# Optimization experiments

Measured on AMD Instinct MI355X. Metric: run time of the kernel, lower is better.

The kernel has to match this reference:

```python
import jax, jax.numpy as jnp
import numpy as np

MEM_DIM = 1024
N_CHILD = 16384

def _linear_params(key, out_dim, in_dim):
    kw, kb = jax.random.split(key)
    bound = 1.0 / np.sqrt(in_dim)
    W = jax.random.uniform(kw, (out_dim, in_dim), jnp.float32, -bound, bound)
    b = jax.random.uniform(kb, (out_dim,), jnp.float32, -bound, bound)
    return W, b

def setup_inputs() -> dict:
    key = jax.random.key(0)
    ks = jax.random.split(key, 7)
    child_c = jax.random.normal(ks[0], (N_CHILD, MEM_DIM), jnp.float32)
    child_h = jax.random.normal(ks[1], (N_CHILD, MEM_DIM), jnp.float32)
    child_h_sum = jax.random.normal(ks[2], (MEM_DIM,), jnp.float32)
    W_ih, b_ih = _linear_params(ks[3], MEM_DIM, MEM_DIM)
    W_fh, b_fh = _linear_params(ks[4], MEM_DIM, MEM_DIM)
    W_uh, b_uh = _linear_params(ks[5], MEM_DIM, MEM_DIM)
    W_oh, b_oh = _linear_params(ks[6], MEM_DIM, MEM_DIM)
    return {
        "child_c": child_c, "child_h": child_h, "child_h_sum": child_h_sum,
        "W_ih": W_ih, "b_ih": b_ih, "W_fh": W_fh, "b_fh": b_fh,
        "W_uh": W_uh, "b_uh": b_uh, "W_oh": W_oh, "b_oh": b_oh,
    }

def reference(child_c, child_h, child_h_sum,
              W_ih, b_ih, W_fh, b_fh, W_uh, b_uh, W_oh, b_oh):
    # Gate projections on the summed child hidden state: [mem_dim]
    i = jax.nn.sigmoid(child_h_sum @ W_ih.T + b_ih)
    o = jax.nn.sigmoid(child_h_sum @ W_oh.T + b_oh)
    u = jnp.tanh(child_h_sum @ W_uh.T + b_uh)
    # Per-child forget gates, batched (replaces the Python loop): [N, mem_dim]
    f = jax.nn.sigmoid(child_h @ W_fh.T + b_fh)
    fc = f * child_c                     # [N, mem_dim]
    c = i * u + jnp.sum(fc, axis=0)      # [mem_dim]
    h = o * jnp.tanh(c)                  # [mem_dim]
    return (c, h)
```

## Files before the change

kernel.cpp:

```cpp
#include <hip/hip_runtime.h>
#include <hip/hip_bf16.h>
#include <math.h>

#define MEM_DIM 1024
#define N_CHILD 16384

typedef __bf16 bf16_t;
typedef __bf16 bf16x4 __attribute__((ext_vector_type(4)));
typedef __bf16 bf16x8 __attribute__((ext_vector_type(8)));
typedef float f32x4 __attribute__((ext_vector_type(4)));

__device__ __forceinline__ void async_load16(const bf16_t* g, bf16_t* l) {
    __builtin_amdgcn_global_load_lds(
        (const __attribute__((address_space(1))) unsigned int*)g,
        (__attribute__((address_space(3))) unsigned int*)l,
        16, 0, 0);
}

template<int N> __device__ __forceinline__ void wait_vm() {
    if constexpr (N == 0)      asm volatile("s_waitcnt vmcnt(0)" ::: "memory");
    else if constexpr (N == 4) asm volatile("s_waitcnt vmcnt(4)" ::: "memory");
    else if constexpr (N == 8) asm volatile("s_waitcnt vmcnt(8)" ::: "memory");
}

__device__ __forceinline__ void block_barrier() {
    __builtin_amdgcn_sched_barrier(0);
    asm volatile("" ::: "memory");
    __builtin_amdgcn_s_barrier();
    asm volatile("" ::: "memory");
    __builtin_amdgcn_sched_barrier(0);
}

__global__ __launch_bounds__(256) void prep_kernel(
        const float* __restrict__ child_h, const float* __restrict__ W_fh,
        bf16_t* __restrict__ dst, int n8,
        const float* __restrict__ hsum,
        const float* __restrict__ W_ih, const float* __restrict__ b_ih,
        const float* __restrict__ W_uh, const float* __restrict__ b_uh,
        const float* __restrict__ W_oh, const float* __restrict__ b_oh,
        float* __restrict__ acc_c, float* __restrict__ o_ws) {
    const int tid = threadIdx.x;
    if (blockIdx.x < MEM_DIM) {
        const int j = blockIdx.x;
        const float* wi = W_ih + (size_t)j * MEM_DIM;
        const float* wu = W_uh + (size_t)j * MEM_DIM;
        const float* wo = W_oh + (size_t)j * MEM_DIM;
        float4 h4  = *(const float4*)(hsum + tid * 4);
        float4 wi4 = *(const float4*)(wi + tid * 4);
        float4 wu4 = *(const float4*)(wu + tid * 4);
        float4 wo4 = *(const float4*)(wo + tid * 4);
        float si = wi4.x * h4.x + wi4.y * h4.y + wi4.z * h4.z + wi4.w * h4.w;
        float su = wu4.x * h4.x + wu4.y * h4.y + wu4.z * h4.z + wu4.w * h4.w;
        float so = wo4.x * h4.x + wo4.y * h4.y + wo4.z * h4.z + wo4.w * h4.w;
        for (int off = 32; off > 0; off >>= 1) {
            si += __shfl_down(si, off, 64);
            su += __shfl_down(su, off, 64);
            so += __shfl_down(so, off, 64);
        }
        __shared__ float red[3][4];
        const int wave = tid >> 6, lane = tid & 63;
        if (lane == 0) { red[0][wave] = si; red[1][wave] = su; red[2][wave] = so; }
        __syncthreads();
        if (tid == 0) {
            float ti = red[0][0] + red[0][1] + red[0][2] + red[0][3] + b_ih[j];
            float tu = red[1][0] + red[1][1] + red[1][2] + red[1][3] + b_uh[j];
            float to = red[2][0] + red[2][1] + red[2][2] + red[2][3] + b_oh[j];
            float iv = 1.f / (1.f + expf(-ti));
            float uv = tanhf(tu);
            float ov = 1.f / (1.f + expf(-to));
            acc_c[j] = iv * uv;
            o_ws[j]  = ov;
        }
    } else {
        const int nA8 = (N_CHILD * MEM_DIM) / 8;
        int t = (blockIdx.x - MEM_DIM) * 256 + tid;
        if (t < n8) {
            const float* s = (t < nA8) ? (child_h + (size_t)t * 8)
                                       : (W_fh + (size_t)(t - nA8) * 8);
            float4 a = *(const float4*)s;
            float4 b = *(const float4*)(s + 4);
            bf16x8 o = { (bf16_t)a.x, (bf16_t)a.y, (bf16_t)a.z, (bf16_t)a.w,
                         (bf16_t)b.x, (bf16_t)b.y, (bf16_t)b.z, (bf16_t)b.w };
            *(bf16x8*)(dst + (size_t)t * 8) = o;
        }
    }
}


__device__ __forceinline__ void stage_slot(const bf16_t* __restrict__ gbase,
                                           int row0, int s, bf16_t* lds_slot,
                                           int tid) {
    const int wave = tid >> 6;
    const int rr   = tid >> 2;
    const int cf   = ((tid & 3) ^ (rr & 3)) * 8;
#pragma unroll
    for (int i = 0; i < 2; ++i) {
        const bf16_t* src = gbase + (size_t)(row0 + i * 128 + rr) * MEM_DIM
                          + s * 32 + cf;
        bf16_t* dst = lds_slot + i * 4096 + wave * 512;
        async_load16(src, dst);
    }
}

template<int VMN, bool STG>
__device__ __forceinline__ void do_slice(
        int s, bf16_t* ldsA, bf16_t* ldsB,
        const bf16_t* __restrict__ hbf, const bf16_t* __restrict__ wbf,
        int n0, int j0, int tid, int wr, int wc, int q, int cl,
        f32x4 (&acc)[8][4]) {
    const int m = s & 3;
    const int koff  = (q ^ (cl & 3)) * 8;
    const int abase = m * 8192 + (wr * 128 + cl) * 32 + koff;
    const int bbase = m * 8192 + (wc * 64  + cl) * 32 + koff;
    bf16x8 af[8], bfr[2];

#pragma unroll
    for (int mt = 0; mt < 8; ++mt)
        af[mt] = *(const bf16x8*)(&ldsA[abase + mt * 512]);
#pragma unroll
    for (int nt = 0; nt < 2; ++nt)
        bfr[nt] = *(const bf16x8*)(&ldsB[bbase + nt * 512]);
    if (STG) stage_slot(hbf, n0, s + 3, ldsA + ((s + 3) & 3) * 8192, tid);
    block_barrier();
    asm volatile("s_waitcnt lgkmcnt(0)" ::: "memory");
    __builtin_amdgcn_sched_barrier(0);
    __builtin_amdgcn_s_setprio(1);
#pragma unroll
    for (int mt = 0; mt < 8; ++mt) {
        acc[mt][0] = __builtin_amdgcn_mfma_f32_16x16x32_bf16(af[mt], bfr[0], acc[mt][0], 0, 0, 0);
        acc[mt][1] = __builtin_amdgcn_mfma_f32_16x16x32_bf16(af[mt], bfr[1], acc[mt][1], 0, 0, 0);
    }
    __builtin_amdgcn_s_setprio(0);
    block_barrier();

#pragma unroll
    for (int nt = 0; nt < 2; ++nt)
        bfr[nt] = *(const bf16x8*)(&ldsB[bbase + (2 + nt) * 512]);
    if (STG) stage_slot(wbf, j0, s + 3, ldsB + ((s + 3) & 3) * 8192, tid);
    if constexpr (VMN >= 0) wait_vm<VMN>();
    block_barrier();
    asm volatile("s_waitcnt lgkmcnt(0)" ::: "memory");
    __builtin_amdgcn_sched_barrier(0);
    __builtin_amdgcn_s_setprio(1);
#pragma unroll
    for (int mt = 0; mt < 8; ++mt) {
        acc[mt][2] = __builtin_amdgcn_mfma_f32_16x16x32_bf16(af[mt], bfr[0], acc[mt][2], 0, 0, 0);
        acc[mt][3] = __builtin_amdgcn_mfma_f32_16x16x32_bf16(af[mt], bfr[1], acc[mt][3], 0, 0, 0);
    }
    __builtin_amdgcn_s_setprio(0);
    block_barrier();
}

__global__ __launch_bounds__(512, 2) void gemm8_kernel(
        const bf16_t* __restrict__ hbf, const bf16_t* __restrict__ wbf,
        const float* __restrict__ child_c, const float* __restrict__ b_fh,
        float* __restrict__ acc_part) {
    __shared__ __align__(1024) bf16_t ldsA[4 * 8192];
    __shared__ __align__(1024) bf16_t ldsB[4 * 8192];
    __shared__ float sred[256];

    const int tid  = threadIdx.x;
    const int lane = tid & 63;
    const int wave = tid >> 6;
    const int wr = wave >> 2;
    const int wc = wave & 3;
    const int q  = lane >> 4;
    const int cl = lane & 15;

    const int b   = blockIdx.x;
    const int xcd = b & 7;
    const int l   = b >> 3;
    const int jt  = l & 3;
    const int ntl = l >> 2;
    const int j0  = jt * 256;
    const int n0  = (xcd * 8 + ntl) * 256;
    const int part = xcd * 8 + ntl;

    f32x4 acc[8][4];
#pragma unroll
    for (int a = 0; a < 8; ++a)
#pragma unroll
        for (int c = 0; c < 4; ++c) acc[a][c] = (f32x4)0.0f;

#pragma unroll
    for (int s = 0; s < 3; ++s) {
        stage_slot(hbf, n0, s, ldsA + (s & 3) * 8192, tid);
        stage_slot(wbf, j0, s, ldsB + (s & 3) * 8192, tid);
    }
    wait_vm<8>();
    block_barrier();

#pragma unroll 1
    for (int s = 0; s < 29; ++s)
        do_slice<8, true>(s, ldsA, ldsB, hbf, wbf, n0, j0, tid, wr, wc, q, cl, acc);
    do_slice<4,  false>(29, ldsA, ldsB, hbf, wbf, n0, j0, tid, wr, wc, q, cl, acc);
    do_slice<0,  false>(30, ldsA, ldsB, hbf, wbf, n0, j0, tid, wr, wc, q, cl, acc);
    do_slice<-1, false>(31, ldsA, ldsB, hbf, wbf, n0, j0, tid, wr, wc, q, cl, acc);

    float colsum[4] = {0.f, 0.f, 0.f, 0.f};
#pragma unroll
    for (int nt = 0; nt < 4; ++nt) {
        const int j = j0 + wc * 64 + nt * 16 + cl;
        const float bias = b_fh[j];
#pragma unroll
        for (int mt = 0; mt < 8; ++mt) {
            const int nrow = n0 + wr * 128 + mt * 16 + q * 4;
            const float* ccp = child_c + (size_t)nrow * MEM_DIM + j;
#pragma unroll
            for (int rr = 0; rr < 4; ++rr) {
                float sv = acc[mt][nt][rr] + bias;
                float fg = 1.0f / (1.0f + __expf(-sv));
                colsum[nt] += fg * ccp[(size_t)rr * MEM_DIM];
            }
        }
        colsum[nt] += __shfl_xor(colsum[nt], 16, 64);
        colsum[nt] += __shfl_xor(colsum[nt], 32, 64);
    }
    if (tid < 256) sred[tid] = 0.0f;
    __syncthreads();
    if (q == 0) {
#pragma unroll
        for (int nt = 0; nt < 4; ++nt)
            atomicAdd(&sred[wc * 64 + nt * 16 + cl], colsum[nt]);
    }
    __syncthreads();
    if (tid < 256)
        acc_part[(size_t)part * MEM_DIM + j0 + tid] = sred[tid];
}

__global__ __launch_bounds__(256) void finalize2(
        const float* __restrict__ acc_part, const float* __restrict__ iu_ws,
        const float* __restrict__ o_ws, float* __restrict__ out) {
    const int j = blockIdx.x * 256 + threadIdx.x;
    float s = iu_ws[j];
#pragma unroll 8
    for (int p = 0; p < 64; ++p)
        s += acc_part[(size_t)p * MEM_DIM + j];
    out[j] = s;
    out[MEM_DIM + j] = o_ws[j] * tanhf(s);
}

__global__ void gates_kernel(const float* __restrict__ hsum,
                             const float* __restrict__ W_ih, const float* __restrict__ b_ih,
                             const float* __restrict__ W_uh, const float* __restrict__ b_uh,
                             const float* __restrict__ W_oh, const float* __restrict__ b_oh,
                             float* __restrict__ acc_c, float* __restrict__ o_ws) {
    const int j = blockIdx.x;
    const int tid = threadIdx.x;
    const float* wi = W_ih + (size_t)j * MEM_DIM;
    const float* wu = W_uh + (size_t)j * MEM_DIM;
    const float* wo = W_oh + (size_t)j * MEM_DIM;
    float si = 0.f, su = 0.f, so = 0.f;
    for (int k = tid; k < MEM_DIM; k += 256) {
        float hv = hsum[k];
        si += wi[k] * hv;
        su += wu[k] * hv;
        so += wo[k] * hv;
    }
    for (int off = 32; off > 0; off >>= 1) {
        si += __shfl_down(si, off, 64);
        su += __shfl_down(su, off, 64);
        so += __shfl_down(so, off, 64);
    }
    __shared__ float red[3][4];
    const int wave = tid >> 6, lane = tid & 63;
    if (lane == 0) { red[0][wave] = si; red[1][wave] = su; red[2][wave] = so; }
    __syncthreads();
    if (tid == 0) {
        float ti = red[0][0] + red[0][1] + red[0][2] + red[0][3] + b_ih[j];
        float tu = red[1][0] + red[1][1] + red[1][2] + red[1][3] + b_uh[j];
        float to = red[2][0] + red[2][1] + red[2][2] + red[2][3] + b_oh[j];
        acc_c[j] = (1.f / (1.f + expf(-ti))) * tanhf(tu);
        o_ws[j]  = 1.f / (1.f + expf(-to));
    }
}

#define LDS_STRIDE 40
__global__ __launch_bounds__(256) void fused_gemm_f32(
        const float* __restrict__ child_h, const float* __restrict__ child_c,
        const float* __restrict__ W_fh, const float* __restrict__ b_fh,
        float* __restrict__ acc_c) {
    __shared__ __align__(16) bf16_t sA[128 * LDS_STRIDE];
    __shared__ __align__(16) bf16_t sB[128 * LDS_STRIDE];
    __shared__ float sred[128];
    const int tid = threadIdx.x, lane = tid & 63, wave = tid >> 6;
    const int wr = wave >> 1, wc = wave & 1;
    const int j0 = blockIdx.x * 128, n0 = blockIdx.y * 128;
    const int q = lane >> 4, cl = lane & 15;
    f32x4 acc[4][4];
#pragma unroll
    for (int a = 0; a < 4; a++)
#pragma unroll
        for (int c = 0; c < 4; c++) acc[a][c] = (f32x4)0.0f;
    for (int k0 = 0; k0 < MEM_DIM; k0 += 32) {
#pragma unroll
        for (int i = 0; i < 4; i++) {
            int f = tid + i * 256, row = f >> 3, col = (f & 7) * 4;
            float4 va = *(const float4*)(child_h + (size_t)(n0 + row) * MEM_DIM + k0 + col);
            float4 vb = *(const float4*)(W_fh    + (size_t)(j0 + row) * MEM_DIM + k0 + col);
            bf16x4 ba = { (bf16_t)va.x, (bf16_t)va.y, (bf16_t)va.z, (bf16_t)va.w };
            bf16x4 bb = { (bf16_t)vb.x, (bf16_t)vb.y, (bf16_t)vb.z, (bf16_t)vb.w };
            *(bf16x4*)(&sA[row * LDS_STRIDE + col]) = ba;
            *(bf16x4*)(&sB[row * LDS_STRIDE + col]) = bb;
        }
        __syncthreads();
        bf16x8 af[4], bfr[4];
#pragma unroll
        for (int mt = 0; mt < 4; mt++) {
            af[mt]  = *(const bf16x8*)(&sA[(wr * 64 + mt * 16 + cl) * LDS_STRIDE + q * 8]);
            bfr[mt] = *(const bf16x8*)(&sB[(wc * 64 + mt * 16 + cl) * LDS_STRIDE + q * 8]);
        }
#pragma unroll
        for (int mt = 0; mt < 4; mt++)
#pragma unroll
            for (int nt = 0; nt < 4; nt++)
                acc[mt][nt] = __builtin_amdgcn_mfma_f32_16x16x32_bf16(af[mt], bfr[nt], acc[mt][nt], 0, 0, 0);
        __syncthreads();
    }
    if (tid < 128) sred[tid] = 0.0f;
    __syncthreads();
    float colsum[4] = {0.f, 0.f, 0.f, 0.f};
#pragma unroll
    for (int nt = 0; nt < 4; nt++) {
        const int col = j0 + wc * 64 + nt * 16 + cl;
        const float bias = b_fh[col];
#pragma unroll
        for (int mt = 0; mt < 4; mt++)
#pragma unroll
            for (int r = 0; r < 4; r++) {
                const int row = n0 + wr * 64 + mt * 16 + q * 4 + r;
                float s = acc[mt][nt][r] + bias;
                float fg = 1.0f / (1.0f + __expf(-s));
                colsum[nt] += fg * child_c[(size_t)row * MEM_DIM + col];
            }
        colsum[nt] += __shfl_xor(colsum[nt], 16, 64);
        colsum[nt] += __shfl_xor(colsum[nt], 32, 64);
    }
    if (q == 0)
#pragma unroll
        for (int nt = 0; nt < 4; nt++)
            atomicAdd(&sred[wc * 64 + nt * 16 + cl], colsum[nt]);
    __syncthreads();
    if (tid < 128) atomicAdd(&acc_c[j0 + tid], sred[tid]);
}

__global__ void finalize_old(const float* __restrict__ acc_c,
                             const float* __restrict__ o_ws,
                             float* __restrict__ out) {
    int t = blockIdx.x * 256 + threadIdx.x;
    if (t < MEM_DIM) {
        float cv = acc_c[t];
        float hv = o_ws[t] * tanhf(cv);
        out[t] = cv;
        out[MEM_DIM + t] = hv;
    }
}

extern "C" void kernel_launch(void* const* d_in, const int* in_sizes, int n_in,
                              void* d_out, int out_size, void* d_ws, size_t ws_size,
                              hipStream_t stream) {
    const float* child_c = (const float*)d_in[0];
    const float* child_h = (const float*)d_in[1];
    const float* hsum    = (const float*)d_in[2];
    const float* W_ih    = (const float*)d_in[3];
    const float* b_ih    = (const float*)d_in[4];
    const float* W_fh    = (const float*)d_in[5];
    const float* b_fh    = (const float*)d_in[6];
    const float* W_uh    = (const float*)d_in[7];
    const float* b_uh    = (const float*)d_in[8];
    const float* W_oh    = (const float*)d_in[9];
    const float* b_oh    = (const float*)d_in[10];
    float* out   = (float*)d_out;

    float* acc_c = (float*)d_ws;
    float* o_ws  = acc_c + MEM_DIM;
    const size_t HBF_OFF   = 8192;
    const size_t HBF_BYTES = (size_t)N_CHILD * MEM_DIM * 2;
    const size_t WBF_BYTES = (size_t)MEM_DIM * MEM_DIM * 2;
    const size_t PART_BYTES = (size_t)64 * MEM_DIM * 4;
    const size_t NEED = HBF_OFF + HBF_BYTES + WBF_BYTES + PART_BYTES;

    if (ws_size >= NEED) {
        bf16_t* hbf = (bf16_t*)((char*)d_ws + HBF_OFF);
        bf16_t* wbf = hbf + (size_t)N_CHILD * MEM_DIM;
        float* acc_part = (float*)(wbf + (size_t)MEM_DIM * MEM_DIM);
        const int n8 = (N_CHILD * MEM_DIM + MEM_DIM * MEM_DIM) / 8;
        const int cvtBlocks = (n8 + 255) / 256;
        prep_kernel<<<MEM_DIM + cvtBlocks, 256, 0, stream>>>(
            child_h, W_fh, hbf, n8,
            hsum, W_ih, b_ih, W_uh, b_uh, W_oh, b_oh, acc_c, o_ws);
        gemm8_kernel<<<256, 512, 0, stream>>>(hbf, wbf, child_c, b_fh, acc_part);
        finalize2<<<MEM_DIM / 256, 256, 0, stream>>>(acc_part, acc_c, o_ws, out);
    } else {
        gates_kernel<<<MEM_DIM, 256, 0, stream>>>(hsum, W_ih, b_ih, W_uh, b_uh,
                                                  W_oh, b_oh, acc_c, o_ws);
        dim3 grid(MEM_DIM / 128, N_CHILD / 128);
        fused_gemm_f32<<<grid, 256, 0, stream>>>(child_h, child_c, W_fh, b_fh, acc_c);
        finalize_old<<<(MEM_DIM + 255) / 256, 256, 0, stream>>>(acc_c, o_ws, out);
    }
}
```

Before: 218.4 us.

## Collapse per-slice barriers into one and issue all prefetches upfront

Each K-slice now issues both A and B async prefetches at the start, loads all B fragments at once, and runs all 32 MFMAs in a single block. The four block barriers and the explicit sched_barriers per slice are replaced with a single s_barrier at the end. This is meant to cut synchronization and scheduling fences that serialized the MFMA work. The trade-offs are more live registers (four B fragments) and less control over how the compiler interleaves LDS reads and MFMAs.

Measured after the change: 226.0 us. 1.03x slower.

```diff
diff --git a/kernel.cpp b/kernel.cpp
--- a/kernel.cpp
+++ b/kernel.cpp
@@ -21,14 +21,6 @@
     if constexpr (N == 0)      asm volatile("s_waitcnt vmcnt(0)" ::: "memory");
     else if constexpr (N == 4) asm volatile("s_waitcnt vmcnt(4)" ::: "memory");
     else if constexpr (N == 8) asm volatile("s_waitcnt vmcnt(8)" ::: "memory");
-}
-
-__device__ __forceinline__ void block_barrier() {
-    __builtin_amdgcn_sched_barrier(0);
-    asm volatile("" ::: "memory");
-    __builtin_amdgcn_s_barrier();
-    asm volatile("" ::: "memory");
-    __builtin_amdgcn_sched_barrier(0);
 }
 
 __global__ __launch_bounds__(256) void prep_kernel(
@@ -108,47 +100,32 @@
         const bf16_t* __restrict__ hbf, const bf16_t* __restrict__ wbf,
         int n0, int j0, int tid, int wr, int wc, int q, int cl,
         f32x4 (&acc)[8][4]) {
+    if constexpr (STG) {
+        stage_slot(hbf, n0, s + 3, ldsA + ((s + 3) & 3) * 8192, tid);
+        stage_slot(wbf, j0, s + 3, ldsB + ((s + 3) & 3) * 8192, tid);
+    }
     const int m = s & 3;
     const int koff  = (q ^ (cl & 3)) * 8;
     const int abase = m * 8192 + (wr * 128 + cl) * 32 + koff;
     const int bbase = m * 8192 + (wc * 64  + cl) * 32 + koff;
-    bf16x8 af[8], bfr[2];
-
+    bf16x8 af[8], bfr[4];
 #pragma unroll
     for (int mt = 0; mt < 8; ++mt)
         af[mt] = *(const bf16x8*)(&ldsA[abase + mt * 512]);
 #pragma unroll
-    for (int nt = 0; nt < 2; ++nt)
+    for (int nt = 0; nt < 4; ++nt)
         bfr[nt] = *(const bf16x8*)(&ldsB[bbase + nt * 512]);
-    if (STG) stage_slot(hbf, n0, s + 3, ldsA + ((s + 3) & 3) * 8192, tid);
-    block_barrier();
-    asm volatile("s_waitcnt lgkmcnt(0)" ::: "memory");
-    __builtin_amdgcn_sched_barrier(0);
     __builtin_amdgcn_s_setprio(1);
 #pragma unroll
-    for (int mt = 0; mt < 8; ++mt) {
-        acc[mt][0] = __builtin_amdgcn_mfma_f32_16x16x32_bf16(af[mt], bfr[0], acc[mt][0], 0, 0, 0);
-        acc[mt][1] = __builtin_amdgcn_mfma_f32_16x16x32_bf16(af[mt], bfr[1], acc[mt][1], 0, 0, 0);
-    }
+    for (int mt = 0; mt < 8; ++mt)
+#pragma unroll
+        for (int nt = 0; nt < 4; ++nt)
+            acc[mt][nt] = __builtin_amdgcn_mfma_f32_16x16x32_bf16(
+                af[mt], bfr[nt], acc[mt][nt], 0, 0, 0);
     __builtin_amdgcn_s_setprio(0);
-    block_barrier();
-
-#pragma unroll
-    for (int nt = 0; nt < 2; ++nt)
-        bfr[nt] = *(const bf16x8*)(&ldsB[bbase + (2 + nt) * 512]);
-    if (STG) stage_slot(wbf, j0, s + 3, ldsB + ((s + 3) & 3) * 8192, tid);
     if constexpr (VMN >= 0) wait_vm<VMN>();
-    block_barrier();
-    asm volatile("s_waitcnt lgkmcnt(0)" ::: "memory");
-    __builtin_amdgcn_sched_barrier(0);
-    __builtin_amdgcn_s_setprio(1);
-#pragma unroll
-    for (int mt = 0; mt < 8; ++mt) {
-        acc[mt][2] = __builtin_amdgcn_mfma_f32_16x16x32_bf16(af[mt], bfr[0], acc[mt][2], 0, 0, 0);
-        acc[mt][3] = __builtin_amdgcn_mfma_f32_16x16x32_bf16(af[mt], bfr[1], acc[mt][3], 0, 0, 0);
-    }
-    __builtin_amdgcn_s_setprio(0);
-    block_barrier();
+    __builtin_amdgcn_s_barrier();
+    asm volatile("" ::: "memory");
 }
 
 __global__ __launch_bounds__(512, 2) void gemm8_kernel(
@@ -188,7 +165,8 @@
         stage_slot(wbf, j0, s, ldsB + (s & 3) * 8192, tid);
     }
     wait_vm<8>();
-    block_barrier();
+    __builtin_amdgcn_s_barrier();
+    asm volatile("" ::: "memory");
 
 #pragma unroll 1
     for (int s = 0; s < 29; ++s)
```
